# Kernel optimization log

Measured on AMD Instinct MI355X. Metric: run time of the kernel, lower is better.

Reference implementation:

```python
import jax, jax.numpy as jnp
import numpy as np

N_EMBD = 64
N_HEAD = 4
HEAD_DIM = N_EMBD // N_HEAD  # 16


def setup_inputs() -> dict:
    key = jax.random.key(0)
    ks = jax.random.split(key, 4)
    B, T = 1024, 128
    x = jax.random.normal(ks[0], (B, T, N_EMBD), dtype=jnp.float32)
    W_attn = jax.random.normal(ks[1], (N_EMBD, 3 * N_EMBD), dtype=jnp.float32) * (1.0 / np.sqrt(N_EMBD))
    b_attn = jnp.zeros((3 * N_EMBD,), dtype=jnp.float32)
    W_proj = jax.random.normal(ks[2], (N_EMBD, N_EMBD), dtype=jnp.float32) * (1.0 / np.sqrt(N_EMBD))
    b_proj = jnp.zeros((N_EMBD,), dtype=jnp.float32)
    return {"x": x, "W_attn": W_attn, "b_attn": b_attn, "W_proj": W_proj, "b_proj": b_proj}


def reference(x, W_attn, b_attn, W_proj, b_proj):
    B, T, C = x.shape
    qkv = x @ W_attn + b_attn                      # [B,T,3C]
    q, k, v = jnp.split(qkv, 3, axis=-1)
    # [B,T,C] -> [B,H,T,D]
    q = q.reshape(B, T, N_HEAD, HEAD_DIM).transpose(0, 2, 1, 3)
    k = k.reshape(B, T, N_HEAD, HEAD_DIM).transpose(0, 2, 1, 3)
    v = v.reshape(B, T, N_HEAD, HEAD_DIM).transpose(0, 2, 1, 3)
    att = jnp.einsum('bhtd,bhsd->bhts', q, k) * (HEAD_DIM ** -0.5)  # [B,H,T,T]
    causal = jnp.tril(jnp.ones((T, T), dtype=bool))
    att = jnp.where(causal[None, None], att, -jnp.inf)
    att = jax.nn.softmax(att, axis=-1)
    # dropout is identity in eval mode (reference uses eval semantics)
    y = jnp.einsum('bhts,bhsd->bhtd', att, v)       # [B,H,T,D]
    y = y.transpose(0, 2, 1, 3).reshape(B, T, C)
    return y @ W_proj + b_proj
```

## Files before the change

### kernel.cpp

```cpp
#include <hip/hip_runtime.h>
#include <hip/hip_fp16.h>

#define NTH 512

typedef __attribute__((ext_vector_type(4))) _Float16 f16x4;
typedef __attribute__((ext_vector_type(8))) _Float16 f16x8;
typedef __attribute__((ext_vector_type(4))) float f32x4;

union U16x8 { uint4 u; f16x8 h; };
union U16x4 { uint2 u; f16x4 h; };

static __device__ __forceinline__ unsigned pk2(float a, float b) {
    union { __half2 h; unsigned u; } v;
    v.h = __floats2half2_rn(a, b);
    return v.u;
}
static __device__ __forceinline__ f16x4 pk4(f32x4 v) {
    U16x4 r; r.u = make_uint2(pk2(v[0], v[1]), pk2(v[2], v[3]));
    return r.h;
}
static __device__ __forceinline__ f16x8 ld2b64(const _Float16* p) {
    uint2 lo = *reinterpret_cast<const uint2*>(p);
    uint2 hi = *reinterpret_cast<const uint2*>(p + 4);
    U16x8 r; r.u = make_uint4(lo.x, lo.y, hi.x, hi.y);
    return r.h;
}
static __device__ __forceinline__ f16x8 w_frag(const float* __restrict__ p, int stride, float scale) {
    f16x8 f;
    #pragma unroll
    for (int j = 0; j < 8; ++j) f[j] = (_Float16)(p[j * stride] * scale);
    return f;
}

template<int N0, int N1, int N2, int N3, int NKV>
static __device__ __forceinline__ void wave_attn(
    const _Float16* __restrict__ sx, _Float16* __restrict__ sO,
    const f16x8* wq, const f16x8* wk, const f16x8* wv,
    float4 bq, float4 bk, float bv, int lc, int lg, int h)
{
    constexpr int Ns[4] = {N0, N1, N2, N3};
    f16x4 Kf[NKV], Vf[NKV], Qf[4];

    #pragma unroll
    for (int M = 0; M < NKV; ++M) {
        f16x8 xf0 = *reinterpret_cast<const f16x8*>(sx + (16 * M + lc) * 72 + 8 * lg);
        f16x8 xf1 = *reinterpret_cast<const f16x8*>(sx + (16 * M + lc) * 72 + 32 + 8 * lg);

        f32x4 ka = (f32x4){bk.x, bk.y, bk.z, bk.w};
        ka = __builtin_amdgcn_mfma_f32_16x16x32_f16(wk[0], xf0, ka, 0, 0, 0);
        ka = __builtin_amdgcn_mfma_f32_16x16x32_f16(wk[1], xf1, ka, 0, 0, 0);
        Kf[M] = pk4(ka);

        f32x4 va = (f32x4){bv, bv, bv, bv};
        va = __builtin_amdgcn_mfma_f32_16x16x32_f16(xf0, wv[0], va, 0, 0, 0);
        va = __builtin_amdgcn_mfma_f32_16x16x32_f16(xf1, wv[1], va, 0, 0, 0);
        Vf[M] = pk4(va);

        int u = (M == N0) ? 0 : (M == N1) ? 1 : (M == N2) ? 2 : (M == N3) ? 3 : -1;
        if (u >= 0) {
            f32x4 qa = (f32x4){bq.x, bq.y, bq.z, bq.w};
            qa = __builtin_amdgcn_mfma_f32_16x16x32_f16(wq[0], xf0, qa, 0, 0, 0);
            qa = __builtin_amdgcn_mfma_f32_16x16x32_f16(wq[1], xf1, qa, 0, 0, 0);
            Qf[u] = pk4(qa);
        }
    }

    f32x4 Of[4];
    float l[4];
    #pragma unroll
    for (int u = 0; u < 4; ++u) { Of[u] = (f32x4){0.f, 0.f, 0.f, 0.f}; l[u] = 0.f; }

    #pragma unroll
    for (int st = 0; st < NKV; ++st) {
        #pragma unroll
        for (int u = 0; u < 4; ++u) {
            if (st > Ns[u]) continue;
            f32x4 z = (f32x4){0.f, 0.f, 0.f, 0.f};
            f32x4 sf = __builtin_amdgcn_mfma_f32_16x16x16f16(Kf[st], Qf[u], z, 0, 0, 0);
            float e[4];
            #pragma unroll
            for (int j = 0; j < 4; ++j) {
                float sv = sf[j];
                if (st == Ns[u]) sv = (4 * lg + j <= lc) ? sv : -1e30f;
                e[j] = __expf(sv);
            }
            l[u] += (e[0] + e[1]) + (e[2] + e[3]);
            f32x4 ef = (f32x4){e[0], e[1], e[2], e[3]};
            Of[u] = __builtin_amdgcn_mfma_f32_16x16x16f16(Vf[st], pk4(ef), Of[u], 0, 0, 0);
        }
    }

    #pragma unroll
    for (int u = 0; u < 4; ++u) {
        float lu = l[u];
        lu += __shfl_xor(lu, 16);
        lu += __shfl_xor(lu, 32);
        float inv = __fdividef(1.0f, lu);
        uint2 ou = make_uint2(pk2(Of[u][0] * inv, Of[u][1] * inv),
                              pk2(Of[u][2] * inv, Of[u][3] * inv));
        *reinterpret_cast<uint2*>(sO + (16 * Ns[u] + lc) * 76 + 16 * h + 4 * lg) = ou;
    }
}

__global__ __launch_bounds__(NTH, 4)
void csa_fused(const float* __restrict__ x, const float* __restrict__ Wa,
               const float* __restrict__ ba, const float* __restrict__ Wp,
               const float* __restrict__ bp, float* __restrict__ out)
{
    __shared__ _Float16 sx[128 * 72];
    __shared__ _Float16 sO[128 * 76];

    const int b    = blockIdx.x;
    const int tid  = threadIdx.x;
    const int lane = tid & 63;
    const int w    = tid >> 6;
    const int lc   = lane & 15;
    const int lg   = lane >> 4;
    const int h    = w & 3;
    const int p    = w >> 2;

    const float* __restrict__ xb = x + (size_t)b * 8192;

    #pragma unroll
    for (int e = 0; e < 4; ++e) {
        int f = tid + NTH * e;
        int r = f >> 4, c = (f & 15) << 2;
        float4 v4 = *reinterpret_cast<const float4*>(xb + r * 64 + c);
        U16x4 u; u.u = make_uint2(pk2(v4.x, v4.y), pk2(v4.z, v4.w));
        *reinterpret_cast<f16x4*>(sx + r * 72 + c) = u.h;
    }

    f16x8 wq[2], wk[2], wv[2];
    #pragma unroll
    for (int kk = 0; kk < 2; ++kk) {
        const float* wa_k = Wa + (size_t)(32 * kk + 8 * lg) * 192;
        wq[kk] = w_frag(wa_k + 16 * h + lc,       192, 0.25f);
        wk[kk] = w_frag(wa_k + 64 + 16 * h + lc,  192, 1.0f);
        wv[kk] = w_frag(wa_k + 128 + 16 * h + lc, 192, 1.0f);
    }
    float4 bq = *reinterpret_cast<const float4*>(ba + 16 * h + 4 * lg);
    bq.x *= 0.25f; bq.y *= 0.25f; bq.z *= 0.25f; bq.w *= 0.25f;
    const float4 bk = *reinterpret_cast<const float4*>(ba + 64 + 16 * h + 4 * lg);
    const float  bv = ba[128 + 16 * h + lc];

    __syncthreads();

    if (p == 0)
        wave_attn<0, 3, 4, 7, 8>(sx, sO, wq, wk, wv, bq, bk, bv, lc, lg, h);
    else
        wave_attn<1, 2, 5, 6, 7>(sx, sO, wq, wk, wv, bq, bk, bv, lc, lg, h);

    const int m  = w >> 1;
    const int n0 = 4 * (w & 1);
    f16x8 af[2];
    #pragma unroll
    for (int kk = 0; kk < 2; ++kk)
        af[kk] = w_frag(Wp + (size_t)(32 * kk + 8 * lg) * 64 + 16 * m + lc, 64, 1.0f);
    const float4 bia = *reinterpret_cast<const float4*>(bp + 16 * m + 4 * lg);

    __syncthreads();

    {
        f32x4 dacc[4];
        #pragma unroll
        for (int i = 0; i < 4; ++i) dacc[i] = (f32x4){bia.x, bia.y, bia.z, bia.w};

        #pragma unroll
        for (int kk = 0; kk < 2; ++kk) {
            #pragma unroll
            for (int i = 0; i < 4; ++i) {
                f16x8 bf = ld2b64(sO + (16 * (n0 + i) + lc) * 76 + 32 * kk + 8 * lg);
                dacc[i] = __builtin_amdgcn_mfma_f32_16x16x32_f16(af[kk], bf, dacc[i], 0, 0, 0);
            }
        }
        #pragma unroll
        for (int i = 0; i < 4; ++i) {
            int t = 16 * (n0 + i) + lc;
            *reinterpret_cast<float4*>(out + (size_t)b * 8192 + t * 64 + 16 * m + 4 * lg) =
                make_float4(dacc[i][0], dacc[i][1], dacc[i][2], dacc[i][3]);
        }
    }
}

extern "C" void kernel_launch(void* const* d_in, const int* in_sizes, int n_in,
                              void* d_out, int out_size, void* d_ws, size_t ws_size,
                              hipStream_t stream) {
    const float* x  = (const float*)d_in[0];
    const float* Wa = (const float*)d_in[1];
    const float* ba = (const float*)d_in[2];
    const float* Wp = (const float*)d_in[3];
    const float* bp = (const float*)d_in[4];
    float* out = (float*)d_out;

    const int B = in_sizes[0] / 8192;

    csa_fused<<<B, NTH, 0, stream>>>(x, Wa, ba, Wp, bp, out);
}
```

Before: 25.60 us.

## Process two batches per block and overlap next x staging with projection

Each block now handles two batch elements in sequence. The x fragments and weights are loaded once per block, and the next batch's x is staged into shared memory while the output projection of the current batch runs. A second sO buffer lets the projection read one buffer while the next attention pass writes the other. This halves the grid to 512 blocks, which may lower occupancy and parallelism on a 256-CU device, and it raises LDS use per block.

```diff
diff --git a/kernel.cpp b/kernel.cpp
--- a/kernel.cpp
+++ b/kernel.cpp
@@ -2,6 +2,7 @@
 #include <hip/hip_fp16.h>
 
 #define NTH 512
+#define NB  2
 
 typedef __attribute__((ext_vector_type(4))) _Float16 f16x4;
 typedef __attribute__((ext_vector_type(8))) _Float16 f16x8;
@@ -102,15 +103,26 @@
     }
 }
 
+static __device__ __forceinline__ void stage_x(const float* __restrict__ xb,
+                                               _Float16* __restrict__ sx, int tid) {
+    #pragma unroll
+    for (int e = 0; e < 4; ++e) {
+        int f = tid + NTH * e;
+        int r = f >> 4, c = (f & 15) << 2;
+        float4 v4 = *reinterpret_cast<const float4*>(xb + r * 64 + c);
+        U16x4 u; u.u = make_uint2(pk2(v4.x, v4.y), pk2(v4.z, v4.w));
+        *reinterpret_cast<f16x4*>(sx + r * 72 + c) = u.h;
+    }
+}
+
 __global__ __launch_bounds__(NTH, 4)
 void csa_fused(const float* __restrict__ x, const float* __restrict__ Wa,
                const float* __restrict__ ba, const float* __restrict__ Wp,
                const float* __restrict__ bp, float* __restrict__ out)
 {
     __shared__ _Float16 sx[128 * 72];
-    __shared__ _Float16 sO[128 * 76];
-
-    const int b    = blockIdx.x;
+    __shared__ _Float16 sO[NB][128 * 76];
+
     const int tid  = threadIdx.x;
     const int lane = tid & 63;
     const int w    = tid >> 6;
@@ -119,16 +131,7 @@
     const int h    = w & 3;
     const int p    = w >> 2;
 
-    const float* __restrict__ xb = x + (size_t)b * 8192;
-
-    #pragma unroll
-    for (int e = 0; e < 4; ++e) {
-        int f = tid + NTH * e;
-        int r = f >> 4, c = (f & 15) << 2;
-        float4 v4 = *reinterpret_cast<const float4*>(xb + r * 64 + c);
-        U16x4 u; u.u = make_uint2(pk2(v4.x, v4.y), pk2(v4.z, v4.w));
-        *reinterpret_cast<f16x4*>(sx + r * 72 + c) = u.h;
-    }
+    const size_t bbase = (size_t)blockIdx.x * NB * 8192;
 
     f16x8 wq[2], wk[2], wv[2];
     #pragma unroll
@@ -143,42 +146,54 @@
     const float4 bk = *reinterpret_cast<const float4*>(ba + 64 + 16 * h + 4 * lg);
     const float  bv = ba[128 + 16 * h + lc];
 
-    __syncthreads();
-
-    if (p == 0)
-        wave_attn<0, 3, 4, 7, 8>(sx, sO, wq, wk, wv, bq, bk, bv, lc, lg, h);
-    else
-        wave_attn<1, 2, 5, 6, 7>(sx, sO, wq, wk, wv, bq, bk, bv, lc, lg, h);
-
     const int m  = w >> 1;
     const int n0 = 4 * (w & 1);
-    f16x8 af[2];
-    #pragma unroll
-    for (int kk = 0; kk < 2; ++kk)
-        af[kk] = w_frag(Wp + (size_t)(32 * kk + 8 * lg) * 64 + 16 * m + lc, 64, 1.0f);
-    const float4 bia = *reinterpret_cast<const float4*>(bp + 16 * m + 4 * lg);
-
+
+    stage_x(x + bbase, sx, tid);
     __syncthreads();
 
-    {
-        f32x4 dacc[4];
+    #pragma unroll
+    for (int i = 0; i < NB; ++i) {
+        if (p == 0)
+            wave_attn<0, 3, 4, 7, 8>(sx, sO[i], wq, wk, wv, bq, bk, bv, lc, lg, h);
+        else
+            wave_attn<1, 2, 5, 6, 7>(sx, sO[i], wq, wk, wv, bq, bk, bv, lc, lg, h);
+
+        f16x8 af[2];
         #pragma unroll
-        for (int i = 0; i < 4; ++i) dacc[i] = (f32x4){bia.x, bia.y, bia.z, bia.w};
-
-        #pragma unroll
-        for (int kk = 0; kk < 2; ++kk) {
-            #pragma unroll
-            for (int i = 0; i < 4; ++i) {
-                f16x8 bf = ld2b64(sO + (16 * (n0 + i) + lc) * 76 + 32 * kk + 8 * lg);
-                dacc[i] = __builtin_amdgcn_mfma_f32_16x16x32_f16(af[kk], bf, dacc[i], 0, 0, 0);
+        for (int kk = 0; kk < 2; ++kk)
+            af[kk] = w_frag(Wp + (size_t)(32 * kk + 8 * lg) * 64 + 16 * m + lc, 64, 1.0f);
+        const float4 bia = *reinterpret_cast<const float4*>(bp + 16 * m + 4 * lg);
+
+        __syncthreads();
+
+        if (i + 1 < NB)
+            stage_x(x + bbase + (size_t)(i + 1) * 8192, sx, tid);
+
+        {
+            f32x4 dacc[4];
+            #pragma unroll
+            for (int t = 0; t < 4; ++t) dacc[t] = (f32x4){bia.x, bia.y, bia.z, bia.w};
+
+            #pragma unroll
+            for (int kk = 0; kk < 2; ++kk) {
+                #pragma unroll
+                for (int t = 0; t < 4; ++t) {
+                    f16x8 bf = ld2b64(sO[i] + (16 * (n0 + t) + lc) * 76 + 32 * kk + 8 * lg);
+                    dacc[t] = __builtin_amdgcn_mfma_f32_16x16x32_f16(af[kk], bf, dacc[t], 0, 0, 0);
+                }
+            }
+            float* ob = out + bbase + (size_t)i * 8192;
+            #pragma unroll
+            for (int t = 0; t < 4; ++t) {
+                int tt = 16 * (n0 + t) + lc;
+                *reinterpret_cast<float4*>(ob + tt * 64 + 16 * m + 4 * lg) =
+                    make_float4(dacc[t][0], dacc[t][1], dacc[t][2], dacc[t][3]);
             }
         }
-        #pragma unroll
-        for (int i = 0; i < 4; ++i) {
-            int t = 16 * (n0 + i) + lc;
-            *reinterpret_cast<float4*>(out + (size_t)b * 8192 + t * 64 + 16 * m + 4 * lg) =
-                make_float4(dacc[i][0], dacc[i][1], dacc[i][2], dacc[i][3]);
-        }
+
+        if (i + 1 < NB)
+            __syncthreads();
     }
 }
 
@@ -194,5 +209,5 @@
 
     const int B = in_sizes[0] / 8192;
 
-    csa_fused<<<B, NTH, 0, stream>>>(x, Wa, ba, Wp, bp, out);
-}
+    csa_fused<<<B / NB, NTH, 0, stream>>>(x, Wa, ba, Wp, bp, out);
+}
```

After: 36.24 us. 41.6% more time.

## Use one wave per head and compute K/V projections once per block

Applied to the files above, without the earlier changes.

The block drops from 512 to 256 threads, so each wave now handles one head over all query tiles instead of two waves per head each handling half the tiles. Previously both waves of a head recomputed the full K and V projections. Now each wave computes K, V and Q once and runs both causal tile groups itself, which removes the duplicate projection MFMAs. The cost is more registers per wave (Q, K and V arrays of 8 each) and fewer waves per block. That may reduce latency hiding unless occupancy rises through more resident blocks.

```diff
diff --git a/kernel.cpp b/kernel.cpp
--- a/kernel.cpp
+++ b/kernel.cpp
@@ -1,7 +1,7 @@
 #include <hip/hip_runtime.h>
 #include <hip/hip_fp16.h>
 
-#define NTH 512
+#define NTH 256
 
 typedef __attribute__((ext_vector_type(4))) _Float16 f16x4;
 typedef __attribute__((ext_vector_type(8))) _Float16 f16x8;
@@ -33,37 +33,12 @@
 }
 
 template<int N0, int N1, int N2, int N3, int NKV>
-static __device__ __forceinline__ void wave_attn(
-    const _Float16* __restrict__ sx, _Float16* __restrict__ sO,
-    const f16x8* wq, const f16x8* wk, const f16x8* wv,
-    float4 bq, float4 bk, float bv, int lc, int lg, int h)
+static __device__ __forceinline__ void attn_quad(
+    const f16x4* __restrict__ Kf, const f16x4* __restrict__ Vf,
+    const f16x4* __restrict__ Qf, _Float16* __restrict__ sO,
+    int lc, int lg, int h)
 {
     constexpr int Ns[4] = {N0, N1, N2, N3};
-    f16x4 Kf[NKV], Vf[NKV], Qf[4];
-
-    #pragma unroll
-    for (int M = 0; M < NKV; ++M) {
-        f16x8 xf0 = *reinterpret_cast<const f16x8*>(sx + (16 * M + lc) * 72 + 8 * lg);
-        f16x8 xf1 = *reinterpret_cast<const f16x8*>(sx + (16 * M + lc) * 72 + 32 + 8 * lg);
-
-        f32x4 ka = (f32x4){bk.x, bk.y, bk.z, bk.w};
-        ka = __builtin_amdgcn_mfma_f32_16x16x32_f16(wk[0], xf0, ka, 0, 0, 0);
-        ka = __builtin_amdgcn_mfma_f32_16x16x32_f16(wk[1], xf1, ka, 0, 0, 0);
-        Kf[M] = pk4(ka);
-
-        f32x4 va = (f32x4){bv, bv, bv, bv};
-        va = __builtin_amdgcn_mfma_f32_16x16x32_f16(xf0, wv[0], va, 0, 0, 0);
-        va = __builtin_amdgcn_mfma_f32_16x16x32_f16(xf1, wv[1], va, 0, 0, 0);
-        Vf[M] = pk4(va);
-
-        int u = (M == N0) ? 0 : (M == N1) ? 1 : (M == N2) ? 2 : (M == N3) ? 3 : -1;
-        if (u >= 0) {
-            f32x4 qa = (f32x4){bq.x, bq.y, bq.z, bq.w};
-            qa = __builtin_amdgcn_mfma_f32_16x16x32_f16(wq[0], xf0, qa, 0, 0, 0);
-            qa = __builtin_amdgcn_mfma_f32_16x16x32_f16(wq[1], xf1, qa, 0, 0, 0);
-            Qf[u] = pk4(qa);
-        }
-    }
 
     f32x4 Of[4];
     float l[4];
@@ -76,7 +51,7 @@
         for (int u = 0; u < 4; ++u) {
             if (st > Ns[u]) continue;
             f32x4 z = (f32x4){0.f, 0.f, 0.f, 0.f};
-            f32x4 sf = __builtin_amdgcn_mfma_f32_16x16x16f16(Kf[st], Qf[u], z, 0, 0, 0);
+            f32x4 sf = __builtin_amdgcn_mfma_f32_16x16x16f16(Kf[st], Qf[Ns[u]], z, 0, 0, 0);
             float e[4];
             #pragma unroll
             for (int j = 0; j < 4; ++j) {
@@ -116,13 +91,12 @@
     const int w    = tid >> 6;
     const int lc   = lane & 15;
     const int lg   = lane >> 4;
-    const int h    = w & 3;
-    const int p    = w >> 2;
+    const int h    = w;
 
     const float* __restrict__ xb = x + (size_t)b * 8192;
 
     #pragma unroll
-    for (int e = 0; e < 4; ++e) {
+    for (int e = 0; e < 8; ++e) {
         int f = tid + NTH * e;
         int r = f >> 4, c = (f & 15) << 2;
         float4 v4 = *reinterpret_cast<const float4*>(xb + r * 64 + c);
@@ -145,13 +119,32 @@
 
     __syncthreads();
 
-    if (p == 0)
-        wave_attn<0, 3, 4, 7, 8>(sx, sO, wq, wk, wv, bq, bk, bv, lc, lg, h);
-    else
-        wave_attn<1, 2, 5, 6, 7>(sx, sO, wq, wk, wv, bq, bk, bv, lc, lg, h);
+    f16x4 Kf[8], Vf[8], Qf[8];
+    #pragma unroll
+    for (int M = 0; M < 8; ++M) {
+        f16x8 xf0 = *reinterpret_cast<const f16x8*>(sx + (16 * M + lc) * 72 + 8 * lg);
+        f16x8 xf1 = *reinterpret_cast<const f16x8*>(sx + (16 * M + lc) * 72 + 32 + 8 * lg);
 
-    const int m  = w >> 1;
-    const int n0 = 4 * (w & 1);
+        f32x4 ka = (f32x4){bk.x, bk.y, bk.z, bk.w};
+        ka = __builtin_amdgcn_mfma_f32_16x16x32_f16(wk[0], xf0, ka, 0, 0, 0);
+        ka = __builtin_amdgcn_mfma_f32_16x16x32_f16(wk[1], xf1, ka, 0, 0, 0);
+        Kf[M] = pk4(ka);
+
+        f32x4 va = (f32x4){bv, bv, bv, bv};
+        va = __builtin_amdgcn_mfma_f32_16x16x32_f16(xf0, wv[0], va, 0, 0, 0);
+        va = __builtin_amdgcn_mfma_f32_16x16x32_f16(xf1, wv[1], va, 0, 0, 0);
+        Vf[M] = pk4(va);
+
+        f32x4 qa = (f32x4){bq.x, bq.y, bq.z, bq.w};
+        qa = __builtin_amdgcn_mfma_f32_16x16x32_f16(wq[0], xf0, qa, 0, 0, 0);
+        qa = __builtin_amdgcn_mfma_f32_16x16x32_f16(wq[1], xf1, qa, 0, 0, 0);
+        Qf[M] = pk4(qa);
+    }
+
+    attn_quad<0, 3, 4, 7, 8>(Kf, Vf, Qf, sO, lc, lg, h);
+    attn_quad<1, 2, 5, 6, 7>(Kf, Vf, Qf, sO, lc, lg, h);
+
+    const int m = w;
     f16x8 af[2];
     #pragma unroll
     for (int kk = 0; kk < 2; ++kk)
@@ -161,23 +154,23 @@
     __syncthreads();
 
     {
-        f32x4 dacc[4];
+        f32x4 dacc[8];
         #pragma unroll
-        for (int i = 0; i < 4; ++i) dacc[i] = (f32x4){bia.x, bia.y, bia.z, bia.w};
+        for (int t = 0; t < 8; ++t) dacc[t] = (f32x4){bia.x, bia.y, bia.z, bia.w};
 
         #pragma unroll
         for (int kk = 0; kk < 2; ++kk) {
             #pragma unroll
-            for (int i = 0; i < 4; ++i) {
-                f16x8 bf = ld2b64(sO + (16 * (n0 + i) + lc) * 76 + 32 * kk + 8 * lg);
-                dacc[i] = __builtin_amdgcn_mfma_f32_16x16x32_f16(af[kk], bf, dacc[i], 0, 0, 0);
+            for (int t = 0; t < 8; ++t) {
+                f16x8 bf = ld2b64(sO + (16 * t + lc) * 76 + 32 * kk + 8 * lg);
+                dacc[t] = __builtin_amdgcn_mfma_f32_16x16x32_f16(af[kk], bf, dacc[t], 0, 0, 0);
             }
         }
         #pragma unroll
-        for (int i = 0; i < 4; ++i) {
-            int t = 16 * (n0 + i) + lc;
-            *reinterpret_cast<float4*>(out + (size_t)b * 8192 + t * 64 + 16 * m + 4 * lg) =
-                make_float4(dacc[i][0], dacc[i][1], dacc[i][2], dacc[i][3]);
+        for (int t = 0; t < 8; ++t) {
+            int tt = 16 * t + lc;
+            *reinterpret_cast<float4*>(out + (size_t)b * 8192 + tt * 64 + 16 * m + 4 * lg) =
+                make_float4(dacc[t][0], dacc[t][1], dacc[t][2], dacc[t][3]);
         }
     }
 }
```

Result: faster. 24.83 us (-3.0%).
